# Performance work log

Hardware: AMD Instinct MI355X
Metric: run time of the kernel (lower is better)

Reference implementation:

```python
import jax, jax.numpy as jnp
import numpy as np

B, T, I, H = 1024, 96, 256, 1024


def _lin_params(key, fan_in, fan_out):
    kw, kb = jax.random.split(key)
    s = 1.0 / np.sqrt(fan_in)
    W = jax.random.uniform(kw, (fan_in, fan_out), jnp.float32, -s, s)
    b = jax.random.uniform(kb, (fan_out,), jnp.float32, -s, s)
    return W, b


def setup_inputs() -> dict:
    key = jax.random.key(0)
    ks = jax.random.split(key, 16)
    x = jax.random.normal(ks[0], (B, T, I), jnp.float32)
    mask = (jax.random.uniform(ks[1], (B, T, I)) > 0.2).astype(jnp.float32)
    delta = jax.random.uniform(ks[2], (B, T, I), jnp.float32)
    noise = jax.random.normal(ks[3], (B, T, I), jnp.float32) * 0.01
    d = {"x": x, "mask": mask, "delta": delta, "noise": noise}
    # encoder params
    d["enc_Wtd"], d["enc_btd"] = _lin_params(ks[4], I, H)
    d["enc_Wr"], d["enc_br"] = _lin_params(ks[5], H + I, H)
    d["enc_Wmu"], d["enc_bmu"] = _lin_params(ks[6], H + I, H)
    d["enc_Whh"], d["enc_bhh"] = _lin_params(ks[7], H + I, H)
    # latent + decoder-input projections
    d["z_W"], d["z_b"] = _lin_params(ks[8], H, H)
    d["di_W"], d["di_b"] = _lin_params(ks[9], H, I)
    # decoder params
    d["dec_Wtd"], d["dec_btd"] = _lin_params(ks[10], I, H)
    d["dec_Wr"], d["dec_br"] = _lin_params(ks[11], H + I, H)
    d["dec_Wmu"], d["dec_bmu"] = _lin_params(ks[12], H + I, H)
    d["dec_Whh"], d["dec_bhh"] = _lin_params(ks[13], H + I, H)
    d["reg_W"], d["reg_b"] = _lin_params(ks[14], H, I)
    return d


def _grui_cell(h, x_t, d_t, Wtd, btd, Wr, br, Wmu, bmu, Whh, bhh):
    # temporal decay gate: exp(-relu(Lin(delta_t)))
    beta = jnp.exp(-jax.nn.relu(d_t @ Wtd + btd))  # [B,H]
    h = beta * h
    hx = jnp.concatenate([h, x_t], axis=1)          # [B,H+I]
    r = jax.nn.sigmoid(hx @ Wr + br)
    mu = jax.nn.sigmoid(hx @ Wmu + bmu)
    rhx = jnp.concatenate([r * h, x_t], axis=1)
    h_hat = jnp.tanh(rhx @ Whh + bhh)
    return (1.0 - mu) * h + mu * h_hat


def reference(x, mask, delta, noise,
              enc_Wtd, enc_btd, enc_Wr, enc_br, enc_Wmu, enc_bmu, enc_Whh, enc_bhh,
              z_W, z_b, di_W, di_b,
              dec_Wtd, dec_btd, dec_Wr, dec_br, dec_Wmu, dec_bmu, dec_Whh, dec_bhh,
              reg_W, reg_b):
    xin = x * mask + noise                            # [B,T,I]
    xs = jnp.swapaxes(xin, 0, 1)                      # [T,B,I]
    ds = jnp.swapaxes(delta, 0, 1)                    # [T,B,I]
    h0 = jnp.zeros((x.shape[0], enc_Wr.shape[1]), x.dtype)

    # ---- encoder scan (dropout = identity in eval) ----
    def enc_step(h, td):
        x_t, d_t = td
        h = _grui_cell(h, x_t, d_t, enc_Wtd, enc_btd, enc_Wr, enc_br,
                       enc_Wmu, enc_bmu, enc_Whh, enc_bhh)
        return h, None

    h_enc, _ = jax.lax.scan(enc_step, h0, (xs, ds))

    z = h_enc @ z_W + z_b
    dec_in = z @ di_W + di_b                          # [B,I]

    # ---- decoder scan: carries (h, x_t), emits x_t after reg_out ----
    def dec_step(carry, d_t):
        h, x_t = carry
        h = _grui_cell(h, x_t, d_t, dec_Wtd, dec_btd, dec_Wr, dec_br,
                       dec_Wmu, dec_bmu, dec_Whh, dec_bhh)
        x_next = jnp.tanh(h @ reg_W + reg_b)
        return (h, x_next), x_next

    _, outs = jax.lax.scan(dec_step, (h0, dec_in), ds)  # outs: [T,B,I]
    return jnp.swapaxes(outs, 0, 1)                     # [B,T,I]
```

## Files before the change

kernel.cpp:

```cpp
#include <hip/hip_runtime.h>
#include <cstdint>
#include <cstddef>

#define B_ 1024
#define T_ 96
#define I_ 256
#define H_ 1024

typedef unsigned short u16;
typedef __attribute__((ext_vector_type(8))) short short8;
typedef __attribute__((ext_vector_type(4))) float f32x4;
typedef __attribute__((ext_vector_type(4))) unsigned int u32x4;

__device__ __forceinline__ float bf2f(u16 u) {
  union { unsigned int i; float f; } v;
  v.i = ((unsigned int)u) << 16;
  return v.f;
}
__device__ __forceinline__ u16 f2bf(float f) {
  union { float f; unsigned int i; } v;
  v.f = f;
  unsigned int u = v.i;
  return (u16)((u + 0x7FFFu + ((u >> 16) & 1u)) >> 16);
}
// ... 10 lines not shown
  atomicAdd(&cnt, c);
  __syncthreads();
  if (threadIdx.x == 0) *flag = (cnt > 32) ? 1 : 0;
}

__global__ void zero_f32(float* __restrict__ p, int n) {
  int i = blockIdx.x * 256 + threadIdx.x;
  if (i < n) p[i] = 0.f;
}

__global__ void transpose_w(const void* __restrict__ W, u16* __restrict__ Th,
                            u16* __restrict__ Tl, int K, int N,
                            const int* __restrict__ dflag) {
  __shared__ float tile[32][33];
  const int f = *dflag;
  int n0 = blockIdx.x * 32, k0 = blockIdx.y * 32;
  int tx = threadIdx.x, ty = threadIdx.y;
#pragma unroll
  for (int i = ty; i < 32; i += 8) {
    size_t o = (size_t)(k0 + i) * N + n0 + tx;
    tile[i][tx] = f ? ((const float*)W)[o] : bf2f(((const u16*)W)[o]);
  }
  __syncthreads();
#pragma unroll
  for (int i = ty; i < 32; i += 8) {
    float v = tile[tx][i];
    u16 h = f2bf(v);
    size_t o = (size_t)(n0 + i) * K + k0 + tx;
    Th[o] = h;
    Tl[o] = f2bf(v - bf2f(h));
  }
}

__global__ void ew_reg(float* __restrict__ P, const void* __restrict__ bias,
                       float* __restrict__ Xt, void* __restrict__ out, int t,
                       const int* __restrict__ dflag) {
  const int f = *dflag;
  int i = blockIdx.x * 256 + threadIdx.x;
  int col = i & (I_ - 1);
  int row = i >> 8;
  float bv = f ? ((const float*)bias)[col] : bf2f(((const u16*)bias)[col]);
  float v = tanhf(P[i] + bv);
  Xt[i] = v;
  size_t oidx = (size_t)row * (T_ * I_) + (size_t)t * I_ + col;
  if (f) ((float*)out)[oidx] = v;
  else ((u16*)out)[oidx] = f2bf(v);
  P[i] = 0.f;
}

template <int BN, int EPI, int AMODE>
__global__ __launch_bounds__(256) void gemm_k(
    const void* __restrict__ A0, int lda0, int aoff0, int K0,
    const void* __restrict__ Ax, const void* __restrict__ Am,
    const void* __restrict__ An, int lda1, int aoff1,
    const u16* __restrict__ BTh, const u16* __restrict__ BTl, int K, int Ksl,
    const void* __restrict__ bias0, const void* __restrict__ bias1,
    const float* __restrict__ src0, const float* __restrict__ src1,
    float* __restrict__ dst0, int dstr0, float* __restrict__ dst1,
    const int* __restrict__ dflag) {
  __shared__ __align__(16) u16 As_hi[64][40];
  __shared__ __align__(16) u16 As_lo[64][40];
  __shared__ __align__(16) u16 Bs_hi[BN][40];
  __shared__ __align__(16) u16 Bs_lo[BN][40];

  const int f = *dflag;
  const bool alo = (AMODE != 0) || f;

  const int tid = threadIdx.x;
  const int m0 = blockIdx.y * 64;
  const int n0 = blockIdx.x * BN;
  const int kbeg = blockIdx.z * Ksl;
  const int kend = kbeg + Ksl;

  const int w = tid >> 6;
  const int lane = tid & 63;
  const int wx = w & 1, wy = w >> 1;
  const int lr = lane & 15, q = lane >> 4;
  constexpr int NB = BN / 32;

  f32x4 acc[2][NB];
#pragma unroll
  for (int mb = 0; mb < 2; ++mb)
#pragma unroll
    for (int nb = 0; nb < NB; ++nb)
      acc[mb][nb] = (f32x4){0.f, 0.f, 0.f, 0.f};

  const int ar = tid >> 2, ac8 = (tid & 3) * 8;
  const int bn = (BN == 128) ? (tid >> 1) : (tid >> 2);
  const int bc = (BN == 128) ? ((tid & 1) * 16) : ((tid & 3) * 8);

  float av[8];
  u32x4 pbh0, pbh1, pbl0, pbl1;

  auto load_chunk = [&](int kc) {
    if (AMODE == 0) {
      size_t o = (size_t)(m0 + ar) * lda0 + aoff0 + kc + ac8;
      if (f) {
        f32x4 t0 = *(const f32x4*)((const float*)A0 + o);
        f32x4 t1 = *(const f32x4*)((const float*)A0 + o + 4);
#pragma unroll
        for (int j = 0; j < 4; ++j) { av[j] = t0[j]; av[j + 4] = t1[j]; }
      } else {
        union { u32x4 v; u16 s[8]; } t;
        t.v = *(const u32x4*)((const u16*)A0 + o);
#pragma unroll
        for (int j = 0; j < 8; ++j) av[j] = bf2f(t.s[j]);
      }
    } else if (kc < K0) {
      const float* Af = (const float*)A0 + (size_t)(m0 + ar) * lda0 + kc + ac8;
      f32x4 t0 = *(const f32x4*)Af;
      f32x4 t1 = *(const f32x4*)(Af + 4);
#pragma unroll
      for (int j = 0; j < 4; ++j) { av[j] = t0[j]; av[j + 4] = t1[j]; }
    } else if (AMODE == 1) {
      const float* Af = (const float*)Ax + (size_t)(m0 + ar) * lda1 + (kc - K0) + ac8;
      f32x4 t0 = *(const f32x4*)Af;
      f32x4 t1 = *(const f32x4*)(Af + 4);
#pragma unroll
      for (int j = 0; j < 4; ++j) { av[j] = t0[j]; av[j + 4] = t1[j]; }
    } else {
      size_t o = (size_t)(m0 + ar) * lda1 + aoff1 + (kc - K0) + ac8;
      if (f) {
        const float* xp = (const float*)Ax + o;
        const float* mp = (const float*)Am + o;
        const float* np = (const float*)An + o;
        f32x4 x0 = *(const f32x4*)xp, x1 = *(const f32x4*)(xp + 4);
        f32x4 m0v = *(const f32x4*)mp, m1v = *(const f32x4*)(mp + 4);
        f32x4 n0v = *(const f32x4*)np, n1v = *(const f32x4*)(np + 4);
#pragma unroll
        for (int j = 0; j < 4; ++j) {
          av[j] = x0[j] * m0v[j] + n0v[j];
          av[j + 4] = x1[j] * m1v[j] + n1v[j];
        }
      } else {
        union { u32x4 v; u16 s[8]; } ux, um, un;
        ux.v = *(const u32x4*)((const u16*)Ax + o);
        um.v = *(const u32x4*)((const u16*)Am + o);
        un.v = *(const u32x4*)((const u16*)An + o);
#pragma unroll
        for (int j = 0; j < 8; ++j)
          av[j] = bf2f(ux.s[j]) * bf2f(um.s[j]) + bf2f(un.s[j]);
      }
    }
    const u16* Bph = BTh + (size_t)(n0 + bn) * K + kc + bc;
    pbh0 = *(const u32x4*)Bph;
    if (BN == 128) pbh1 = *(const u32x4*)(Bph + 8);
    if (f) {
      const u16* Bpl = BTl + (size_t)(n0 + bn) * K + kc + bc;
      pbl0 = *(const u32x4*)Bpl;
      if (BN == 128) pbl1 = *(const u32x4*)(Bpl + 8);
    }
  };

  load_chunk(kbeg);

  for (int kc = kbeg; kc < kend; kc += 32) {
    {
      union { u16 s[8]; u32x4 v; } ph, pl;
#pragma unroll
      for (int j = 0; j < 8; ++j) {
        u16 h = f2bf(av[j]);
        ph.s[j] = h;
        pl.s[j] = f2bf(av[j] - bf2f(h));
      }
      *(u32x4*)&As_hi[ar][ac8] = ph.v;
      if (alo) *(u32x4*)&As_lo[ar][ac8] = pl.v;
    }
    *(u32x4*)&Bs_hi[bn][bc] = pbh0;
    if (BN == 128) *(u32x4*)&Bs_hi[bn][bc + 8] = pbh1;
    if (f) {
      *(u32x4*)&Bs_lo[bn][bc] = pbl0;
      if (BN == 128) *(u32x4*)&Bs_lo[bn][bc + 8] = pbl1;
    }
    __syncthreads();

    if (kc + 32 < kend) load_chunk(kc + 32);

    short8 ah[2], al[2];
#pragma unroll
    for (int mb = 0; mb < 2; ++mb) {
      ah[mb] = *(const short8*)&As_hi[wy * 32 + mb * 16 + lr][q * 8];
      if (alo) al[mb] = *(const short8*)&As_lo[wy * 32 + mb * 16 + lr][q * 8];
    }
#pragma unroll
    for (int nb = 0; nb < NB; ++nb) {
      short8 bh = *(const short8*)&Bs_hi[wx * (BN / 2) + nb * 16 + lr][q * 8];
#pragma unroll
      for (int mb = 0; mb < 2; ++mb) {
        acc[mb][nb] = __builtin_amdgcn_mfma_f32_16x16x32_bf16(ah[mb], bh, acc[mb][nb], 0, 0, 0);
        if (alo)
          acc[mb][nb] = __builtin_amdgcn_mfma_f32_16x16x32_bf16(al[mb], bh, acc[mb][nb], 0, 0, 0);
      }
      if (f) {
        short8 bl = *(const short8*)&Bs_lo[wx * (BN / 2) + nb * 16 + lr][q * 8];
#pragma unroll
        for (int mb = 0; mb < 2; ++mb)
          acc[mb][nb] = __builtin_amdgcn_mfma_f32_16x16x32_bf16(ah[mb], bl, acc[mb][nb], 0, 0, 0);
      }
    }
    __syncthreads();
  }

  auto bget = [&](const void* b, int c) -> float {
    return f ? ((const float*)b)[c] : bf2f(((const u16*)b)[c]);
  };

#pragma unroll
  for (int mb = 0; mb < 2; ++mb) {
#pragma unroll
    for (int nb = 0; nb < NB; ++nb) {
#pragma unroll
      for (int r = 0; r < 4; ++r) {
        int row = m0 + wy * 32 + mb * 16 + q * 4 + r;
        int col = n0 + wx * (BN / 2) + nb * 16 + lr;
        float p = acc[mb][nb][r];
        if (EPI == 0) {
          dst0[(size_t)row * dstr0 + col] = p + bget(bias0, col);
        } else if (EPI == 1) {
          float tt = p + bget(bias0, col);
          float beta = expf(-fmaxf(tt, 0.f));
          dst0[(size_t)row * H_ + col] = beta * src0[(size_t)row * H_ + col];
        } else if (EPI == 2) {
          if (col < H_) {
            float rr = 1.f / (1.f + expf(-(p + bget(bias0, col))));
            dst0[(size_t)row * H_ + col] = rr * src0[(size_t)row * H_ + col];
          } else {
            int c = col - H_;
            float mu = 1.f / (1.f + expf(-(p + bget(bias1, c))));
            dst1[(size_t)row * H_ + c] = mu;
          }
        } else if (EPI == 3) {
          float hh = tanhf(p + bget(bias0, col));
          float mu = src1[(size_t)row * H_ + col];
          float hs = src0[(size_t)row * H_ + col];
          dst0[(size_t)row * H_ + col] = (1.f - mu) * hs + mu * hh;
        } else if (EPI == 4) {
          atomicAdd(&dst0[(size_t)row * dstr0 + col], p);
        }
      }
    }
  }
}

extern "C" void kernel_launch(void* const* d_in, const int* in_sizes, int n_in,
                              void* d_out, int out_size, void* d_ws, size_t ws_size,
                              hipStream_t stream) {
  const void* x_ = d_in[0];
  const void* mask_ = d_in[1];
  const void* delta_ = d_in[2];
  const void* noise_ = d_in[3];
  const void* eWtd = d_in[4];
  const void* ebtd = d_in[5];
  const void* eWr = d_in[6];
  const void* ebr = d_in[7];
  const void* eWmu = d_in[8];
  const void* ebmu = d_in[9];
  const void* eWhh = d_in[10];
  const void* ebhh = d_in[11];
  const void* zW = d_in[12];
  const void* zb = d_in[13];
  const void* diW = d_in[14];
  const void* dib = d_in[15];
  const void* dWtd = d_in[16];
  const void* dbtd = d_in[17];
  const void* dWr = d_in[18];
  const void* dbr = d_in[19];
  const void* dWmu = d_in[20];
  const void* dbmu = d_in[21];
  const void* dWhh = d_in[22];
  const void* dbhh = d_in[23];
  const void* rW = d_in[24];
  const void* rb = d_in[25];

  char* ws = (char*)d_ws;
  size_t off = 0;
  auto alloc = [&](size_t bytes) -> char* {
    char* p = ws + off;
    off = (off + bytes + 255) & ~(size_t)255;
    return p;
  };
  int* dflag = (int*)alloc(256);
  float* Hb = (float*)alloc((size_t)B_ * H_ * 4);
  float* Hs = (float*)alloc((size_t)B_ * H_ * 4);
  float* RH = (float*)alloc((size_t)B_ * H_ * 4);
  float* MUb = (float*)alloc((size_t)B_ * H_ * 4);
  float* Xt = (float*)alloc((size_t)B_ * I_ * 4);
  float* Pr = (float*)alloc((size_t)B_ * I_ * 4);
  auto wpair = [&](size_t elems, u16** lo) -> u16* {
    u16* hi = (u16*)alloc(elems * 2);
    *lo = (u16*)alloc(elems * 2);
    return hi;
  };
  u16 *eWtdL, *eWrmL, *eWhhL, *zWL, *diWL, *dWtdL, *dWrmL, *dWhhL, *rWL;
  u16* eWtdT = wpair((size_t)H_ * I_, &eWtdL);
  u16* eWrmT = wpair((size_t)2 * H_ * (H_ + I_), &eWrmL);
  u16* eWhhT = wpair((size_t)H_ * (H_ + I_), &eWhhL);
  u16* zWT = wpair((size_t)H_ * H_, &zWL);
  u16* diWT = wpair((size_t)I_ * H_, &diWL);
  u16* dWtdT = wpair((size_t)H_ * I_, &dWtdL);
  u16* dWrmT = wpair((size_t)2 * H_ * (H_ + I_), &dWrmL);
  u16* dWhhT = wpair((size_t)H_ * (H_ + I_), &dWhhL);
  u16* rWT = wpair((size_t)I_ * H_, &rWL);

  detect_dtype<<<1, 256, 0, stream>>>((const u16*)x_, dflag);
  zero_f32<<<(B_ * H_) / 256, 256, 0, stream>>>(Hb, B_ * H_);
  zero_f32<<<(B_ * I_) / 256, 256, 0, stream>>>(Pr, B_ * I_);

  auto tr = [&](const void* W, u16* Th, u16* Tl, int K, int N) {
    transpose_w<<<dim3(N / 32, K / 32), dim3(32, 8), 0, stream>>>(W, Th, Tl, K, N, dflag);
  };
  tr(eWtd, eWtdT, eWtdL, I_, H_);
  tr(eWr, eWrmT, eWrmL, H_ + I_, H_);
  tr(eWmu, eWrmT + (size_t)H_ * (H_ + I_), eWrmL + (size_t)H_ * (H_ + I_), H_ + I_, H_);
  tr(eWhh, eWhhT, eWhhL, H_ + I_, H_);
  tr(zW, zWT, zWL, H_, H_);
  tr(diW, diWT, diWL, H_, I_);
  tr(dWtd, dWtdT, dWtdL, I_, H_);
  tr(dWr, dWrmT, dWrmL, H_ + I_, H_);
  tr(dWmu, dWrmT + (size_t)H_ * (H_ + I_), dWrmL + (size_t)H_ * (H_ + I_), H_ + I_, H_);
  tr(dWhh, dWhhT, dWhhL, H_ + I_, H_);
  tr(rW, rWT, rWL, H_, I_);

  const int GY = B_ / 64;

  for (int t = 0; t < T_; ++t) {
    gemm_k<64, 1, 0><<<dim3(H_ / 64, GY, 1), 256, 0, stream>>>(
        delta_, T_ * I_, t * I_, I_, nullptr, nullptr, nullptr, 0, 0,
        eWtdT, eWtdL, I_, I_, ebtd, nullptr, Hb, nullptr, Hs, H_, nullptr, dflag);
    gemm_k<128, 2, 2><<<dim3((2 * H_) / 128, GY, 1), 256, 0, stream>>>(
        Hs, H_, 0, H_, x_, mask_, noise_, T_ * I_, t * I_,
        eWrmT, eWrmL, H_ + I_, H_ + I_, ebr, ebmu, Hs, nullptr, RH, H_, MUb, dflag);
    gemm_k<64, 3, 2><<<dim3(H_ / 64, GY, 1), 256, 0, stream>>>(
        RH, H_, 0, H_, x_, mask_, noise_, T_ * I_, t * I_,
        eWhhT, eWhhL, H_ + I_, H_ + I_, ebhh, nullptr, Hs, MUb, Hb, H_, nullptr, dflag);
  }

  gemm_k<128, 0, 1><<<dim3(H_ / 128, GY, 1), 256, 0, stream>>>(
      Hb, H_, 0, H_, Hb, nullptr, nullptr, H_, 0,
      zWT, zWL, H_, H_, zb, nullptr, nullptr, nullptr, RH, H_, nullptr, dflag);
  gemm_k<128, 0, 1><<<dim3(I_ / 128, GY, 1), 256, 0, stream>>>(
      RH, H_, 0, H_, RH, nullptr, nullptr, H_, 0,
      diWT, diWL, H_, H_, dib, nullptr, nullptr, nullptr, Xt, I_, nullptr, dflag);
  zero_f32<<<(B_ * H_) / 256, 256, 0, stream>>>(Hb, B_ * H_);

  for (int t = 0; t < T_; ++t) {
    gemm_k<64, 1, 0><<<dim3(H_ / 64, GY, 1), 256, 0, stream>>>(
        delta_, T_ * I_, t * I_, I_, nullptr, nullptr, nullptr, 0, 0,
        dWtdT, dWtdL, I_, I_, dbtd, nullptr, Hb, nullptr, Hs, H_, nullptr, dflag);
    gemm_k<128, 2, 1><<<dim3((2 * H_) / 128, GY, 1), 256, 0, stream>>>(
        Hs, H_, 0, H_, Xt, nullptr, nullptr, I_, 0,
        dWrmT, dWrmL, H_ + I_, H_ + I_, dbr, dbmu, Hs, nullptr, RH, H_, MUb, dflag);
    gemm_k<64, 3, 1><<<dim3(H_ / 64, GY, 1), 256, 0, stream>>>(
        RH, H_, 0, H_, Xt, nullptr, nullptr, I_, 0,
        dWhhT, dWhhL, H_ + I_, H_ + I_, dbhh, nullptr, Hs, MUb, Hb, H_, nullptr, dflag);
    gemm_k<64, 4, 1><<<dim3(I_ / 64, GY, 4), 256, 0, stream>>>(
        Hb, H_, 0, H_, Hb, nullptr, nullptr, H_, 0,
        rWT, rWL, H_, H_ / 4, nullptr, nullptr, nullptr, nullptr, Pr, I_, nullptr, dflag);
    ew_reg<<<(B_ * I_) / 256, 256, 0, stream>>>(Pr, rb, Xt, d_out, t, dflag);
  }
}
```

Baseline: 21.08 ms.

## Precompute decay gates for all timesteps, fuse beta into gate GEMMs, drop split-K reg

Hoists the delta-to-beta projection out of both scans into one large batched GEMM over all B*T rows (when workspace allows), and applies beta inside the r/mu and candidate GEMM loaders and epilogues instead of materialising a decayed hidden state each step. Precomputes the masked-noisy input once, and replaces the split-K atomic regression GEMM plus elementwise tanh kernel with a single GEMM whose epilogue writes the output directly. The GEMM main loop is restructured to double-buffer register prefetch. This removes per-step kernel launches and redundant work, at the cost of a large extra workspace buffer, recomputing beta*h in the loads, and a regression GEMM with fewer blocks.

Result: slower. 23.62 ms (+12.0%).

```diff
diff --git a/kernel.cpp b/kernel.cpp
--- a/kernel.cpp
+++ b/kernel.cpp
@@ -66,31 +66,49 @@
   }
 }
 
-__global__ void ew_reg(float* __restrict__ P, const void* __restrict__ bias,
-                       float* __restrict__ Xt, void* __restrict__ out, int t,
-                       const int* __restrict__ dflag) {
+__global__ void make_xin(const void* __restrict__ x, const void* __restrict__ m,
+                         const void* __restrict__ nz, float* __restrict__ o,
+                         const int* __restrict__ dflag) {
   const int f = *dflag;
-  int i = blockIdx.x * 256 + threadIdx.x;
-  int col = i & (I_ - 1);
-  int row = i >> 8;
-  float bv = f ? ((const float*)bias)[col] : bf2f(((const u16*)bias)[col]);
-  float v = tanhf(P[i] + bv);
-  Xt[i] = v;
-  size_t oidx = (size_t)row * (T_ * I_) + (size_t)t * I_ + col;
-  if (f) ((float*)out)[oidx] = v;
-  else ((u16*)out)[oidx] = f2bf(v);
-  P[i] = 0.f;
-}
-
-template <int BN, int EPI, int AMODE>
+  size_t i = ((size_t)blockIdx.x * 256 + threadIdx.x) * 8;
+  float v[8];
+  if (f) {
+    const float* xp = (const float*)x + i;
+    const float* mp = (const float*)m + i;
+    const float* np = (const float*)nz + i;
+    f32x4 x0 = *(const f32x4*)xp, x1 = *(const f32x4*)(xp + 4);
+    f32x4 m0 = *(const f32x4*)mp, m1 = *(const f32x4*)(mp + 4);
+    f32x4 n0 = *(const f32x4*)np, n1 = *(const f32x4*)(np + 4);
+#pragma unroll
+    for (int j = 0; j < 4; ++j) {
+      v[j] = x0[j] * m0[j] + n0[j];
+      v[j + 4] = x1[j] * m1[j] + n1[j];
+    }
+  } else {
+    union { u32x4 q; u16 s[8]; } ux, um, un;
+    ux.q = *(const u32x4*)((const u16*)x + i);
+    um.q = *(const u32x4*)((const u16*)m + i);
+    un.q = *(const u32x4*)((const u16*)nz + i);
+#pragma unroll
+    for (int j = 0; j < 8; ++j) v[j] = bf2f(ux.s[j]) * bf2f(um.s[j]) + bf2f(un.s[j]);
+  }
+  f32x4 o0, o1;
+#pragma unroll
+  for (int j = 0; j < 4; ++j) { o0[j] = v[j]; o1[j] = v[j + 4]; }
+  *(f32x4*)(o + i) = o0;
+  *(f32x4*)(o + i + 4) = o1;
+}
+
+template <int BN, int EPI, int AH, int AI>
 __global__ __launch_bounds__(256) void gemm_k(
     const void* __restrict__ A0, int lda0, int aoff0, int K0,
     const void* __restrict__ Ax, const void* __restrict__ Am,
     const void* __restrict__ An, int lda1, int aoff1,
-    const u16* __restrict__ BTh, const u16* __restrict__ BTl, int K, int Ksl,
+    const float* Bet, int bstr,
+    const u16* __restrict__ BTh, const u16* __restrict__ BTl, int K,
     const void* __restrict__ bias0, const void* __restrict__ bias1,
-    const float* __restrict__ src0, const float* __restrict__ src1,
-    float* __restrict__ dst0, int dstr0, float* __restrict__ dst1,
+    const float* src0, const float* __restrict__ src1,
+    float* dst0, int dstr0, void* __restrict__ dst1, int tstep,
     const int* __restrict__ dflag) {
   __shared__ __align__(16) u16 As_hi[64][40];
   __shared__ __align__(16) u16 As_lo[64][40];
@@ -98,13 +116,11 @@
   __shared__ __align__(16) u16 Bs_lo[BN][40];
 
   const int f = *dflag;
-  const bool alo = (AMODE != 0) || f;
+  const bool alo = (AH != 0) || f;
 
   const int tid = threadIdx.x;
   const int m0 = blockIdx.y * 64;
   const int n0 = blockIdx.x * BN;
-  const int kbeg = blockIdx.z * Ksl;
-  const int kend = kbeg + Ksl;
 
   const int w = tid >> 6;
   const int lane = tid & 63;
@@ -123,93 +139,101 @@
   const int bn = (BN == 128) ? (tid >> 1) : (tid >> 2);
   const int bc = (BN == 128) ? ((tid & 1) * 16) : ((tid & 3) * 8);
 
-  float av[8];
-  u32x4 pbh0, pbh1, pbl0, pbl1;
-
-  auto load_chunk = [&](int kc) {
-    if (AMODE == 0) {
-      size_t o = (size_t)(m0 + ar) * lda0 + aoff0 + kc + ac8;
-      if (f) {
+  auto load_chunk = [&](int kc, float (&av)[8], u32x4 (&pbh)[2], u32x4 (&pbl)[2]) {
+    if (AI == 0 || kc < K0) {
+      if (AH == 0) {
+        size_t o = (size_t)(m0 + ar) * lda0 + aoff0 + kc + ac8;
+        if (f) {
+          f32x4 t0 = *(const f32x4*)((const float*)A0 + o);
+          f32x4 t1 = *(const f32x4*)((const float*)A0 + o + 4);
+#pragma unroll
+          for (int j = 0; j < 4; ++j) { av[j] = t0[j]; av[j + 4] = t1[j]; }
+        } else {
+          union { u32x4 v; u16 s[8]; } t;
+          t.v = *(const u32x4*)((const u16*)A0 + o);
+#pragma unroll
+          for (int j = 0; j < 8; ++j) av[j] = bf2f(t.s[j]);
+        }
+      } else if (AH == 1) {
+        size_t o = (size_t)(m0 + ar) * lda0 + aoff0 + kc + ac8;
         f32x4 t0 = *(const f32x4*)((const float*)A0 + o);
         f32x4 t1 = *(const f32x4*)((const float*)A0 + o + 4);
 #pragma unroll
         for (int j = 0; j < 4; ++j) { av[j] = t0[j]; av[j + 4] = t1[j]; }
       } else {
-        union { u32x4 v; u16 s[8]; } t;
-        t.v = *(const u32x4*)((const u16*)A0 + o);
-#pragma unroll
-        for (int j = 0; j < 8; ++j) av[j] = bf2f(t.s[j]);
+        size_t ob = (size_t)(m0 + ar) * bstr + kc + ac8;
+        size_t oh = (size_t)(m0 + ar) * H_ + kc + ac8;
+        f32x4 b0 = *(const f32x4*)(Bet + ob);
+        f32x4 b1 = *(const f32x4*)(Bet + ob + 4);
+        f32x4 h0 = *(const f32x4*)((const float*)A0 + oh);
+        f32x4 h1 = *(const f32x4*)((const float*)A0 + oh + 4);
+#pragma unroll
+        for (int j = 0; j < 4; ++j) {
+          av[j] = b0[j] * h0[j];
+          av[j + 4] = b1[j] * h1[j];
+        }
       }
-    } else if (kc < K0) {
-      const float* Af = (const float*)A0 + (size_t)(m0 + ar) * lda0 + kc + ac8;
-      f32x4 t0 = *(const f32x4*)Af;
-      f32x4 t1 = *(const f32x4*)(Af + 4);
-#pragma unroll
-      for (int j = 0; j < 4; ++j) { av[j] = t0[j]; av[j + 4] = t1[j]; }
-    } else if (AMODE == 1) {
-      const float* Af = (const float*)Ax + (size_t)(m0 + ar) * lda1 + (kc - K0) + ac8;
-      f32x4 t0 = *(const f32x4*)Af;
-      f32x4 t1 = *(const f32x4*)(Af + 4);
-#pragma unroll
-      for (int j = 0; j < 4; ++j) { av[j] = t0[j]; av[j + 4] = t1[j]; }
     } else {
-      size_t o = (size_t)(m0 + ar) * lda1 + aoff1 + (kc - K0) + ac8;
-      if (f) {
-        const float* xp = (const float*)Ax + o;
-        const float* mp = (const float*)Am + o;
-        const float* np = (const float*)An + o;
-        f32x4 x0 = *(const f32x4*)xp, x1 = *(const f32x4*)(xp + 4);
-        f32x4 m0v = *(const f32x4*)mp, m1v = *(const f32x4*)(mp + 4);
-        f32x4 n0v = *(const f32x4*)np, n1v = *(const f32x4*)(np + 4);
-#pragma unroll
-        for (int j = 0; j < 4; ++j) {
-          av[j] = x0[j] * m0v[j] + n0v[j];
-          av[j + 4] = x1[j] * m1v[j] + n1v[j];
+      int kk = kc - K0;
+      size_t o = (size_t)(m0 + ar) * lda1 + aoff1 + kk + ac8;
+      if (AI == 1) {
+        f32x4 t0 = *(const f32x4*)((const float*)Ax + o);
+        f32x4 t1 = *(const f32x4*)((const float*)Ax + o + 4);
+#pragma unroll
+        for (int j = 0; j < 4; ++j) { av[j] = t0[j]; av[j + 4] = t1[j]; }
+      } else {
+        if (f) {
+          const float* xp = (const float*)Ax + o;
+          const float* mp = (const float*)Am + o;
+          const float* np = (const float*)An + o;
+          f32x4 x0 = *(const f32x4*)xp, x1 = *(const f32x4*)(xp + 4);
+          f32x4 m0v = *(const f32x4*)mp, m1v = *(const f32x4*)(mp + 4);
+          f32x4 n0v = *(const f32x4*)np, n1v = *(const f32x4*)(np + 4);
+#pragma unroll
+          for (int j = 0; j < 4; ++j) {
+            av[j] = x0[j] * m0v[j] + n0v[j];
+            av[j + 4] = x1[j] * m1v[j] + n1v[j];
+          }
+        } else {
+          union { u32x4 v; u16 s[8]; } ux, um, un;
+          ux.v = *(const u32x4*)((const u16*)Ax + o);
+          um.v = *(const u32x4*)((const u16*)Am + o);
+          un.v = *(const u32x4*)((const u16*)An + o);
+#pragma unroll
+          for (int j = 0; j < 8; ++j)
+            av[j] = bf2f(ux.s[j]) * bf2f(um.s[j]) + bf2f(un.s[j]);
         }
-      } else {
-        union { u32x4 v; u16 s[8]; } ux, um, un;
-        ux.v = *(const u32x4*)((const u16*)Ax + o);
-        um.v = *(const u32x4*)((const u16*)Am + o);
-        un.v = *(const u32x4*)((const u16*)An + o);
-#pragma unroll
-        for (int j = 0; j < 8; ++j)
-          av[j] = bf2f(ux.s[j]) * bf2f(um.s[j]) + bf2f(un.s[j]);
       }
     }
     const u16* Bph = BTh + (size_t)(n0 + bn) * K + kc + bc;
-    pbh0 = *(const u32x4*)Bph;
-    if (BN == 128) pbh1 = *(const u32x4*)(Bph + 8);
+    pbh[0] = *(const u32x4*)Bph;
+    if (BN == 128) pbh[1] = *(const u32x4*)(Bph + 8);
     if (f) {
       const u16* Bpl = BTl + (size_t)(n0 + bn) * K + kc + bc;
-      pbl0 = *(const u32x4*)Bpl;
-      if (BN == 128) pbl1 = *(const u32x4*)(Bpl + 8);
-    }
-  };
-
-  load_chunk(kbeg);
-
-  for (int kc = kbeg; kc < kend; kc += 32) {
-    {
-      union { u16 s[8]; u32x4 v; } ph, pl;
-#pragma unroll
-      for (int j = 0; j < 8; ++j) {
-        u16 h = f2bf(av[j]);
-        ph.s[j] = h;
-        pl.s[j] = f2bf(av[j] - bf2f(h));
-      }
-      *(u32x4*)&As_hi[ar][ac8] = ph.v;
-      if (alo) *(u32x4*)&As_lo[ar][ac8] = pl.v;
-    }
-    *(u32x4*)&Bs_hi[bn][bc] = pbh0;
-    if (BN == 128) *(u32x4*)&Bs_hi[bn][bc + 8] = pbh1;
+      pbl[0] = *(const u32x4*)Bpl;
+      if (BN == 128) pbl[1] = *(const u32x4*)(Bpl + 8);
+    }
+  };
+
+  auto drain = [&](float (&av)[8], u32x4 (&pbh)[2], u32x4 (&pbl)[2]) {
+    union { u16 s[8]; u32x4 v; } ph, pl;
+#pragma unroll
+    for (int j = 0; j < 8; ++j) {
+      u16 h = f2bf(av[j]);
+      ph.s[j] = h;
+      pl.s[j] = f2bf(av[j] - bf2f(h));
+    }
+    *(u32x4*)&As_hi[ar][ac8] = ph.v;
+    if (alo) *(u32x4*)&As_lo[ar][ac8] = pl.v;
+    *(u32x4*)&Bs_hi[bn][bc] = pbh[0];
+    if (BN == 128) *(u32x4*)&Bs_hi[bn][bc + 8] = pbh[1];
     if (f) {
-      *(u32x4*)&Bs_lo[bn][bc] = pbl0;
-      if (BN == 128) *(u32x4*)&Bs_lo[bn][bc + 8] = pbl1;
-    }
-    __syncthreads();
-
-    if (kc + 32 < kend) load_chunk(kc + 32);
-
+      *(u32x4*)&Bs_lo[bn][bc] = pbl[0];
+      if (BN == 128) *(u32x4*)&Bs_lo[bn][bc + 8] = pbl[1];
+    }
+  };
+
+  auto mfma_phase = [&]() {
     short8 ah[2], al[2];
 #pragma unroll
     for (int mb = 0; mb < 2; ++mb) {
@@ -232,7 +256,25 @@
           acc[mb][nb] = __builtin_amdgcn_mfma_f32_16x16x32_bf16(ah[mb], bl, acc[mb][nb], 0, 0, 0);
       }
     }
+  };
+
+  float av0[8], av1[8];
+  u32x4 bh0[2], bl0[2], bh1[2], bl1[2];
+  load_chunk(0, av0, bh0, bl0);
+  if (32 < K) load_chunk(32, av1, bh1, bl1);
+  for (int kc = 0; kc < K; kc += 64) {
+    drain(av0, bh0, bl0);
     __syncthreads();
+    if (kc + 64 < K) load_chunk(kc + 64, av0, bh0, bl0);
+    mfma_phase();
+    __syncthreads();
+    if (kc + 32 < K) {
+      drain(av1, bh1, bl1);
+      __syncthreads();
+      if (kc + 96 < K) load_chunk(kc + 96, av1, bh1, bl1);
+      mfma_phase();
+      __syncthreads();
+    }
   }
 
   auto bget = [&](const void* b, int c) -> float {
@@ -250,26 +292,30 @@
         float p = acc[mb][nb][r];
         if (EPI == 0) {
           dst0[(size_t)row * dstr0 + col] = p + bget(bias0, col);
-        } else if (EPI == 1) {
-          float tt = p + bget(bias0, col);
-          float beta = expf(-fmaxf(tt, 0.f));
-          dst0[(size_t)row * H_ + col] = beta * src0[(size_t)row * H_ + col];
         } else if (EPI == 2) {
           if (col < H_) {
             float rr = 1.f / (1.f + expf(-(p + bget(bias0, col))));
-            dst0[(size_t)row * H_ + col] = rr * src0[(size_t)row * H_ + col];
+            dst0[(size_t)row * H_ + col] =
+                rr * Bet[(size_t)row * bstr + col] * src0[(size_t)row * H_ + col];
           } else {
             int c = col - H_;
             float mu = 1.f / (1.f + expf(-(p + bget(bias1, c))));
-            dst1[(size_t)row * H_ + c] = mu;
+            ((float*)dst1)[(size_t)row * H_ + c] = mu;
           }
         } else if (EPI == 3) {
+          size_t ix = (size_t)row * H_ + col;
           float hh = tanhf(p + bget(bias0, col));
-          float mu = src1[(size_t)row * H_ + col];
-          float hs = src0[(size_t)row * H_ + col];
-          dst0[(size_t)row * H_ + col] = (1.f - mu) * hs + mu * hh;
-        } else if (EPI == 4) {
-          atomicAdd(&dst0[(size_t)row * dstr0 + col], p);
+          float mu = src1[ix];
+          float hs = Bet[(size_t)row * bstr + col] * src0[ix];
+          dst0[ix] = (1.f - mu) * hs + mu * hh;
+        } else if (EPI == 5) {
+          float v = tanhf(p + bget(bias0, col));
+          dst0[(size_t)row * dstr0 + col] = v;
+          size_t ox = (size_t)row * (T_ * I_) + (size_t)tstep * I_ + col;
+          if (f) ((float*)dst1)[ox] = v;
+          else ((u16*)dst1)[ox] = f2bf(v);
+        } else if (EPI == 7) {
+          dst0[(size_t)row * dstr0 + col] = expf(-fmaxf(p + bget(bias0, col), 0.f));
         }
       }
     }
@@ -315,11 +361,10 @@
   };
   int* dflag = (int*)alloc(256);
   float* Hb = (float*)alloc((size_t)B_ * H_ * 4);
-  float* Hs = (float*)alloc((size_t)B_ * H_ * 4);
   float* RH = (float*)alloc((size_t)B_ * H_ * 4);
   float* MUb = (float*)alloc((size_t)B_ * H_ * 4);
   float* Xt = (float*)alloc((size_t)B_ * I_ * 4);
-  float* Pr = (float*)alloc((size_t)B_ * I_ * 4);
+  float* Beta1 = (float*)alloc((size_t)B_ * H_ * 4);
   auto wpair = [&](size_t elems, u16** lo) -> u16* {
     u16* hi = (u16*)alloc(elems * 2);
     *lo = (u16*)alloc(elems * 2);
@@ -335,10 +380,15 @@
   u16* dWrmT = wpair((size_t)2 * H_ * (H_ + I_), &dWrmL);
   u16* dWhhT = wpair((size_t)H_ * (H_ + I_), &dWhhL);
   u16* rWT = wpair((size_t)I_ * H_, &rWL);
+  float* Xin = (float*)alloc((size_t)B_ * T_ * I_ * 4);
+  size_t xin_end = off;
+  float* BetaT = (float*)alloc((size_t)B_ * T_ * H_ * 4);
+  size_t full_end = off;
+  const bool xinT = ws_size >= xin_end;
+  const bool fullT = ws_size >= full_end;
 
   detect_dtype<<<1, 256, 0, stream>>>((const u16*)x_, dflag);
   zero_f32<<<(B_ * H_) / 256, 256, 0, stream>>>(Hb, B_ * H_);
-  zero_f32<<<(B_ * I_) / 256, 256, 0, stream>>>(Pr, B_ * I_);
 
   auto tr = [&](const void* W, u16* Th, u16* Tl, int K, int N) {
     transpose_w<<<dim3(N / 32, K / 32), dim3(32, 8), 0, stream>>>(W, Th, Tl, K, N, dflag);
@@ -355,41 +405,68 @@
   tr(dWhh, dWhhT, dWhhL, H_ + I_, H_);
   tr(rW, rWT, rWL, H_, I_);
 
+  if (xinT)
+    make_xin<<<(B_ * T_ * I_) / (256 * 8), 256, 0, stream>>>(x_, mask_, noise_, Xin, dflag);
+
   const int GY = B_ / 64;
 
+  auto beta_all = [&](const u16* Th, const u16* Tl, const void* bias) {
+    gemm_k<128, 7, 0, 0><<<dim3(H_ / 128, (B_ * T_) / 64), 256, 0, stream>>>(
+        delta_, I_, 0, I_, nullptr, nullptr, nullptr, 0, 0, nullptr, 0,
+        Th, Tl, I_, bias, nullptr, nullptr, nullptr, BetaT, H_, nullptr, 0, dflag);
+  };
+  auto beta_step = [&](const u16* Th, const u16* Tl, const void* bias, int t) {
+    gemm_k<128, 7, 0, 0><<<dim3(H_ / 128, GY), 256, 0, stream>>>(
+        delta_, T_ * I_, t * I_, I_, nullptr, nullptr, nullptr, 0, 0, nullptr, 0,
+        Th, Tl, I_, bias, nullptr, nullptr, nullptr, Beta1, H_, nullptr, 0, dflag);
+  };
+
+  if (fullT) beta_all(eWtdT, eWtdL, ebtd);
   for (int t = 0; t < T_; ++t) {
-    gemm_k<64, 1, 0><<<dim3(H_ / 64, GY, 1), 256, 0, stream>>>(
-        delta_, T_ * I_, t * I_, I_, nullptr, nullptr, nullptr, 0, 0,
-        eWtdT, eWtdL, I_, I_, ebtd, nullptr, Hb, nullptr, Hs, H_, nullptr, dflag);
-    gemm_k<128, 2, 2><<<dim3((2 * H_) / 128, GY, 1), 256, 0, stream>>>(
-        Hs, H_, 0, H_, x_, mask_, noise_, T_ * I_, t * I_,
-        eWrmT, eWrmL, H_ + I_, H_ + I_, ebr, ebmu, Hs, nullptr, RH, H_, MUb, dflag);
-    gemm_k<64, 3, 2><<<dim3(H_ / 64, GY, 1), 256, 0, stream>>>(
-        RH, H_, 0, H_, x_, mask_, noise_, T_ * I_, t * I_,
-        eWhhT, eWhhL, H_ + I_, H_ + I_, ebhh, nullptr, Hs, MUb, Hb, H_, nullptr, dflag);
-  }
-
-  gemm_k<128, 0, 1><<<dim3(H_ / 128, GY, 1), 256, 0, stream>>>(
-      Hb, H_, 0, H_, Hb, nullptr, nullptr, H_, 0,
-      zWT, zWL, H_, H_, zb, nullptr, nullptr, nullptr, RH, H_, nullptr, dflag);
-  gemm_k<128, 0, 1><<<dim3(I_ / 128, GY, 1), 256, 0, stream>>>(
-      RH, H_, 0, H_, RH, nullptr, nullptr, H_, 0,
-      diWT, diWL, H_, H_, dib, nullptr, nullptr, nullptr, Xt, I_, nullptr, dflag);
+    const float* Bet;
+    int bstr;
+    if (fullT) { Bet = BetaT + (size_t)t * H_; bstr = T_ * H_; }
+    else { beta_step(eWtdT, eWtdL, ebtd, t); Bet = Beta1; bstr = H_; }
+    if (xinT)
+      gemm_k<128, 2, 2, 1><<<dim3((2 * H_) / 128, GY), 256, 0, stream>>>(
+          Hb, H_, 0, H_, Xin, nullptr, nullptr, T_ * I_, t * I_, Bet, bstr,
+          eWrmT, eWrmL, H_ + I_, ebr, ebmu, Hb, nullptr, RH, H_, MUb, 0, dflag);
+    else
+      gemm_k<128, 2, 2, 2><<<dim3((2 * H_) / 128, GY), 256, 0, stream>>>(
+          Hb, H_, 0, H_, x_, mask_, noise_, T_ * I_, t * I_, Bet, bstr,
+          eWrmT, eWrmL, H_ + I_, ebr, ebmu, Hb, nullptr, RH, H_, MUb, 0, dflag);
+    if (xinT)
+      gemm_k<64, 3, 1, 1><<<dim3(H_ / 64, GY), 256, 0, stream>>>(
+          RH, H_, 0, H_, Xin, nullptr, nullptr, T_ * I_, t * I_, Bet, bstr,
+          eWhhT, eWhhL, H_ + I_, ebhh, nullptr, Hb, MUb, Hb, H_, nullptr, 0, dflag);
+    else
+      gemm_k<64, 3, 1, 2><<<dim3(H_ / 64, GY), 256, 0, stream>>>(
+          RH, H_, 0, H_, x_, mask_, noise_, T_ * I_, t * I_, Bet, bstr,
+          eWhhT, eWhhL, H_ + I_, ebhh, nullptr, Hb, MUb, Hb, H_, nullptr, 0, dflag);
+  }
+
+  gemm_k<128, 0, 1, 0><<<dim3(H_ / 128, GY), 256, 0, stream>>>(
+      Hb, H_, 0, H_, nullptr, nullptr, nullptr, 0, 0, nullptr, 0,
+      zWT, zWL, H_, zb, nullptr, nullptr, nullptr, RH, H_, nullptr, 0, dflag);
+  gemm_k<128, 0, 1, 0><<<dim3(I_ / 128, GY), 256, 0, stream>>>(
+      RH, H_, 0, H_, nullptr, nullptr, nullptr, 0, 0, nullptr, 0,
+      diWT, diWL, H_, dib, nullptr, nullptr, nullptr, Xt, I_, nullptr, 0, dflag);
   zero_f32<<<(B_ * H_) / 256, 256, 0, stream>>>(Hb, B_ * H_);
 
+  if (fullT) beta_all(dWtdT, dWtdL, dbtd);
   for (int t = 0; t < T_; ++t) {
-    gemm_k<64, 1, 0><<<dim3(H_ / 64, GY, 1), 256, 0, stream>>>(
-        delta_, T_ * I_, t * I_, I_, nullptr, nullptr, nullptr, 0, 0,
-        dWtdT, dWtdL, I_, I_, dbtd, nullptr, Hb, nullptr, Hs, H_, nullptr, dflag);
-    gemm_k<128, 2, 1><<<dim3((2 * H_) / 128, GY, 1), 256, 0, stream>>>(
-        Hs, H_, 0, H_, Xt, nullptr, nullptr, I_, 0,
-        dWrmT, dWrmL, H_ + I_, H_ + I_, dbr, dbmu, Hs, nullptr, RH, H_, MUb, dflag);
-    gemm_k<64, 3, 1><<<dim3(H_ / 64, GY, 1), 256, 0, stream>>>(
-        RH, H_, 0, H_, Xt, nullptr, nullptr, I_, 0,
-        dWhhT, dWhhL, H_ + I_, H_ + I_, dbhh, nullptr, Hs, MUb, Hb, H_, nullptr, dflag);
-    gemm_k<64, 4, 1><<<dim3(I_ / 64, GY, 4), 256, 0, stream>>>(
-        Hb, H_, 0, H_, Hb, nullptr, nullptr, H_, 0,
-        rWT, rWL, H_, H_ / 4, nullptr, nullptr, nullptr, nullptr, Pr, I_, nullptr, dflag);
-    ew_reg<<<(B_ * I_) / 256, 256, 0, stream>>>(Pr, rb, Xt, d_out, t, dflag);
-  }
-}
+    const float* Bet;
+    int bstr;
+    if (fullT) { Bet = BetaT + (size_t)t * H_; bstr = T_ * H_; }
+    else { beta_step(dWtdT, dWtdL, dbtd, t); Bet = Beta1; bstr = H_; }
+    gemm_k<128, 2, 2, 1><<<dim3((2 * H_) / 128, GY), 256, 0, stream>>>(
+        Hb, H_, 0, H_, Xt, nullptr, nullptr, I_, 0, Bet, bstr,
+        dWrmT, dWrmL, H_ + I_, dbr, dbmu, Hb, nullptr, RH, H_, MUb, 0, dflag);
+    gemm_k<64, 3, 1, 1><<<dim3(H_ / 64, GY), 256, 0, stream>>>(
+        RH, H_, 0, H_, Xt, nullptr, nullptr, I_, 0, Bet, bstr,
+        dWhhT, dWhhL, H_ + I_, dbhh, nullptr, Hb, MUb, Hb, H_, nullptr, 0, dflag);
+    gemm_k<64, 5, 1, 0><<<dim3(I_ / 64, GY), 256, 0, stream>>>(
+        Hb, H_, 0, H_, nullptr, nullptr, nullptr, 0, 0, nullptr, 0,
+        rWT, rWL, H_, rb, nullptr, nullptr, nullptr, Xt, I_, d_out, t, dflag);
+  }
+}
```

## Store intermediate activations as pre-split bf16 hi/lo planes for GEMM operands

Applied to the files above, without the earlier changes.

Intermediate activations (scaled hidden state, r*h, decoder input) are now written by GEMM epilogues directly as bf16 hi/lo plane pairs, so the next GEMM copies them straight into shared memory instead of loading fp32 and splitting in the inner loop. A one-time kernel also precomputes x*mask+noise as hi/lo planes for the whole sequence, when workspace allows, which removes the per-step triple loads and FMA. The aim is to cut per-chunk conversion ALU work and halve activation load bytes. It costs extra workspace and an upfront pass over the full input tensor. It also keeps a fallback path for when the workspace is too small.

Measured after the change: 20.11 ms. 4.6% less time.

```diff
diff --git a/kernel.cpp b/kernel.cpp
--- a/kernel.cpp
+++ b/kernel.cpp
@@ -66,8 +66,46 @@
   }
 }
 
+__global__ void make_xin_planes(const void* __restrict__ x, const void* __restrict__ m,
+                                const void* __restrict__ nz, u16* __restrict__ oh,
+                                u16* __restrict__ ol, const int* __restrict__ dflag) {
+  const int f = *dflag;
+  size_t i = ((size_t)blockIdx.x * 256 + threadIdx.x) * 8;
+  float v[8];
+  if (f) {
+    const float* xp = (const float*)x + i;
+    const float* mp = (const float*)m + i;
+    const float* np = (const float*)nz + i;
+    f32x4 x0 = *(const f32x4*)xp, x1 = *(const f32x4*)(xp + 4);
+    f32x4 m0 = *(const f32x4*)mp, m1 = *(const f32x4*)(mp + 4);
+    f32x4 n0 = *(const f32x4*)np, n1 = *(const f32x4*)(np + 4);
+#pragma unroll
+    for (int j = 0; j < 4; ++j) {
+      v[j] = x0[j] * m0[j] + n0[j];
+      v[j + 4] = x1[j] * m1[j] + n1[j];
+    }
+  } else {
+    union { u32x4 q; u16 s[8]; } ux, um, un;
+    ux.q = *(const u32x4*)((const u16*)x + i);
+    um.q = *(const u32x4*)((const u16*)m + i);
+    un.q = *(const u32x4*)((const u16*)nz + i);
+#pragma unroll
+    for (int j = 0; j < 8; ++j) v[j] = bf2f(ux.s[j]) * bf2f(um.s[j]) + bf2f(un.s[j]);
+  }
+  union { u16 s[8]; u32x4 q; } ph, pl;
+#pragma unroll
+  for (int j = 0; j < 8; ++j) {
+    u16 h = f2bf(v[j]);
+    ph.s[j] = h;
+    pl.s[j] = f2bf(v[j] - bf2f(h));
+  }
+  *(u32x4*)(oh + i) = ph.q;
+  *(u32x4*)(ol + i) = pl.q;
+}
+
 __global__ void ew_reg(float* __restrict__ P, const void* __restrict__ bias,
-                       float* __restrict__ Xt, void* __restrict__ out, int t,
+                       u16* __restrict__ XtH, u16* __restrict__ XtL,
+                       void* __restrict__ out, int t,
                        const int* __restrict__ dflag) {
   const int f = *dflag;
   int i = blockIdx.x * 256 + threadIdx.x;
@@ -75,7 +113,9 @@
   int row = i >> 8;
   float bv = f ? ((const float*)bias)[col] : bf2f(((const u16*)bias)[col]);
   float v = tanhf(P[i] + bv);
-  Xt[i] = v;
+  u16 h = f2bf(v);
+  XtH[i] = h;
+  XtL[i] = f2bf(v - bf2f(h));
   size_t oidx = (size_t)row * (T_ * I_) + (size_t)t * I_ + col;
   if (f) ((float*)out)[oidx] = v;
   else ((u16*)out)[oidx] = f2bf(v);
@@ -84,13 +124,16 @@
 
 template <int BN, int EPI, int AMODE>
 __global__ __launch_bounds__(256) void gemm_k(
-    const void* __restrict__ A0, int lda0, int aoff0, int K0,
+    const void* __restrict__ A0, const void* __restrict__ Al, int lda0,
+    int aoff0, int K0,
     const void* __restrict__ Ax, const void* __restrict__ Am,
     const void* __restrict__ An, int lda1, int aoff1,
     const u16* __restrict__ BTh, const u16* __restrict__ BTl, int K, int Ksl,
     const void* __restrict__ bias0, const void* __restrict__ bias1,
     const float* __restrict__ src0, const float* __restrict__ src1,
+    const u16* __restrict__ sph, const u16* __restrict__ spl,
     float* __restrict__ dst0, int dstr0, float* __restrict__ dst1,
+    u16* __restrict__ dph, u16* __restrict__ dpl,
     const int* __restrict__ dflag) {
   __shared__ __align__(16) u16 As_hi[64][40];
   __shared__ __align__(16) u16 As_lo[64][40];
@@ -124,6 +167,7 @@
   const int bc = (BN == 128) ? ((tid & 1) * 16) : ((tid & 3) * 8);
 
   float av[8];
+  u32x4 pah, pal;
   u32x4 pbh0, pbh1, pbl0, pbl1;
 
   auto load_chunk = [&](int kc) {
@@ -135,45 +179,52 @@
 #pragma unroll
         for (int j = 0; j < 4; ++j) { av[j] = t0[j]; av[j + 4] = t1[j]; }
       } else {
-        union { u32x4 v; u16 s[8]; } t;
-        t.v = *(const u32x4*)((const u16*)A0 + o);
-#pragma unroll
-        for (int j = 0; j < 8; ++j) av[j] = bf2f(t.s[j]);
+        pah = *(const u32x4*)((const u16*)A0 + o);
       }
     } else if (kc < K0) {
-      const float* Af = (const float*)A0 + (size_t)(m0 + ar) * lda0 + kc + ac8;
-      f32x4 t0 = *(const f32x4*)Af;
-      f32x4 t1 = *(const f32x4*)(Af + 4);
-#pragma unroll
-      for (int j = 0; j < 4; ++j) { av[j] = t0[j]; av[j + 4] = t1[j]; }
-    } else if (AMODE == 1) {
-      const float* Af = (const float*)Ax + (size_t)(m0 + ar) * lda1 + (kc - K0) + ac8;
-      f32x4 t0 = *(const f32x4*)Af;
-      f32x4 t1 = *(const f32x4*)(Af + 4);
-#pragma unroll
-      for (int j = 0; j < 4; ++j) { av[j] = t0[j]; av[j + 4] = t1[j]; }
+      size_t o = (size_t)(m0 + ar) * lda0 + aoff0 + kc + ac8;
+      if (AMODE == 1 || AMODE == 2) {
+        f32x4 t0 = *(const f32x4*)((const float*)A0 + o);
+        f32x4 t1 = *(const f32x4*)((const float*)A0 + o + 4);
+#pragma unroll
+        for (int j = 0; j < 4; ++j) { av[j] = t0[j]; av[j + 4] = t1[j]; }
+      } else {
+        pah = *(const u32x4*)((const u16*)A0 + o);
+        pal = *(const u32x4*)((const u16*)Al + o);
+      }
     } else {
-      size_t o = (size_t)(m0 + ar) * lda1 + aoff1 + (kc - K0) + ac8;
-      if (f) {
-        const float* xp = (const float*)Ax + o;
-        const float* mp = (const float*)Am + o;
-        const float* np = (const float*)An + o;
-        f32x4 x0 = *(const f32x4*)xp, x1 = *(const f32x4*)(xp + 4);
-        f32x4 m0v = *(const f32x4*)mp, m1v = *(const f32x4*)(mp + 4);
-        f32x4 n0v = *(const f32x4*)np, n1v = *(const f32x4*)(np + 4);
-#pragma unroll
-        for (int j = 0; j < 4; ++j) {
-          av[j] = x0[j] * m0v[j] + n0v[j];
-          av[j + 4] = x1[j] * m1v[j] + n1v[j];
+      int kk = kc - K0;
+      size_t o = (size_t)(m0 + ar) * lda1 + aoff1 + kk + ac8;
+      if (AMODE == 1) {
+        f32x4 t0 = *(const f32x4*)((const float*)Ax + o);
+        f32x4 t1 = *(const f32x4*)((const float*)Ax + o + 4);
+#pragma unroll
+        for (int j = 0; j < 4; ++j) { av[j] = t0[j]; av[j + 4] = t1[j]; }
+      } else if (AMODE == 3) {
+        pah = *(const u32x4*)((const u16*)Ax + o);
+        pal = *(const u32x4*)((const u16*)Am + o);
+      } else {
+        if (f) {
+          const float* xp = (const float*)Ax + o;
+          const float* mp = (const float*)Am + o;
+          const float* np = (const float*)An + o;
+          f32x4 x0 = *(const f32x4*)xp, x1 = *(const f32x4*)(xp + 4);
+          f32x4 m0v = *(const f32x4*)mp, m1v = *(const f32x4*)(mp + 4);
+          f32x4 n0v = *(const f32x4*)np, n1v = *(const f32x4*)(np + 4);
+#pragma unroll
+          for (int j = 0; j < 4; ++j) {
+            av[j] = x0[j] * m0v[j] + n0v[j];
+            av[j + 4] = x1[j] * m1v[j] + n1v[j];
+          }
+        } else {
+          union { u32x4 v; u16 s[8]; } ux, um, un;
+          ux.v = *(const u32x4*)((const u16*)Ax + o);
+          um.v = *(const u32x4*)((const u16*)Am + o);
+          un.v = *(const u32x4*)((const u16*)An + o);
+#pragma unroll
+          for (int j = 0; j < 8; ++j)
+            av[j] = bf2f(ux.s[j]) * bf2f(um.s[j]) + bf2f(un.s[j]);
         }
-      } else {
-        union { u32x4 v; u16 s[8]; } ux, um, un;
-        ux.v = *(const u32x4*)((const u16*)Ax + o);
-        um.v = *(const u32x4*)((const u16*)Am + o);
-        un.v = *(const u32x4*)((const u16*)An + o);
-#pragma unroll
-        for (int j = 0; j < 8; ++j)
-          av[j] = bf2f(ux.s[j]) * bf2f(um.s[j]) + bf2f(un.s[j]);
       }
     }
     const u16* Bph = BTh + (size_t)(n0 + bn) * K + kc + bc;
@@ -186,10 +237,12 @@
     }
   };
 
-  load_chunk(kbeg);
-
-  for (int kc = kbeg; kc < kend; kc += 32) {
-    {
+  auto drain = [&](int kc) {
+    bool plane = (AMODE == 3) || (AMODE == 4 && kc < K0) || (AMODE == 0 && !f);
+    if (plane) {
+      *(u32x4*)&As_hi[ar][ac8] = pah;
+      if (AMODE != 0) *(u32x4*)&As_lo[ar][ac8] = pal;
+    } else {
       union { u16 s[8]; u32x4 v; } ph, pl;
 #pragma unroll
       for (int j = 0; j < 8; ++j) {
@@ -206,6 +259,12 @@
       *(u32x4*)&Bs_lo[bn][bc] = pbl0;
       if (BN == 128) *(u32x4*)&Bs_lo[bn][bc + 8] = pbl1;
     }
+  };
+
+  load_chunk(kbeg);
+
+  for (int kc = kbeg; kc < kend; kc += 32) {
+    drain(kc);
     __syncthreads();
 
     if (kc + 32 < kend) load_chunk(kc + 32);
@@ -237,6 +296,11 @@
 
   auto bget = [&](const void* b, int c) -> float {
     return f ? ((const float*)b)[c] : bf2f(((const u16*)b)[c]);
+  };
+  auto pstore = [&](size_t ix, float v) {
+    u16 h = f2bf(v);
+    dph[ix] = h;
+    dpl[ix] = f2bf(v - bf2f(h));
   };
 
 #pragma unroll
@@ -251,25 +315,29 @@
         if (EPI == 0) {
           dst0[(size_t)row * dstr0 + col] = p + bget(bias0, col);
         } else if (EPI == 1) {
-          float tt = p + bget(bias0, col);
-          float beta = expf(-fmaxf(tt, 0.f));
-          dst0[(size_t)row * H_ + col] = beta * src0[(size_t)row * H_ + col];
+          float beta = expf(-fmaxf(p + bget(bias0, col), 0.f));
+          pstore((size_t)row * H_ + col, beta * src0[(size_t)row * H_ + col]);
         } else if (EPI == 2) {
           if (col < H_) {
+            size_t ix = (size_t)row * H_ + col;
             float rr = 1.f / (1.f + expf(-(p + bget(bias0, col))));
-            dst0[(size_t)row * H_ + col] = rr * src0[(size_t)row * H_ + col];
+            float hs = bf2f(sph[ix]) + bf2f(spl[ix]);
+            pstore(ix, rr * hs);
           } else {
             int c = col - H_;
             float mu = 1.f / (1.f + expf(-(p + bget(bias1, c))));
             dst1[(size_t)row * H_ + c] = mu;
           }
         } else if (EPI == 3) {
+          size_t ix = (size_t)row * H_ + col;
           float hh = tanhf(p + bget(bias0, col));
-          float mu = src1[(size_t)row * H_ + col];
-          float hs = src0[(size_t)row * H_ + col];
-          dst0[(size_t)row * H_ + col] = (1.f - mu) * hs + mu * hh;
+          float mu = src1[ix];
+          float hs = bf2f(sph[ix]) + bf2f(spl[ix]);
+          dst0[ix] = (1.f - mu) * hs + mu * hh;
         } else if (EPI == 4) {
           atomicAdd(&dst0[(size_t)row * dstr0 + col], p);
+        } else if (EPI == 6) {
+          pstore((size_t)row * dstr0 + col, p + bget(bias0, col));
         }
       }
     }
@@ -315,11 +383,15 @@
   };
   int* dflag = (int*)alloc(256);
   float* Hb = (float*)alloc((size_t)B_ * H_ * 4);
-  float* Hs = (float*)alloc((size_t)B_ * H_ * 4);
-  float* RH = (float*)alloc((size_t)B_ * H_ * 4);
   float* MUb = (float*)alloc((size_t)B_ * H_ * 4);
-  float* Xt = (float*)alloc((size_t)B_ * I_ * 4);
+  float* Z = (float*)alloc((size_t)B_ * H_ * 4);
   float* Pr = (float*)alloc((size_t)B_ * I_ * 4);
+  u16* HsH = (u16*)alloc((size_t)B_ * H_ * 2);
+  u16* HsL = (u16*)alloc((size_t)B_ * H_ * 2);
+  u16* RHH = (u16*)alloc((size_t)B_ * H_ * 2);
+  u16* RHL = (u16*)alloc((size_t)B_ * H_ * 2);
+  u16* XtH = (u16*)alloc((size_t)B_ * I_ * 2);
+  u16* XtL = (u16*)alloc((size_t)B_ * I_ * 2);
   auto wpair = [&](size_t elems, u16** lo) -> u16* {
     u16* hi = (u16*)alloc(elems * 2);
     *lo = (u16*)alloc(elems * 2);
@@ -335,6 +407,9 @@
   u16* dWrmT = wpair((size_t)2 * H_ * (H_ + I_), &dWrmL);
   u16* dWhhT = wpair((size_t)H_ * (H_ + I_), &dWhhL);
   u16* rWT = wpair((size_t)I_ * H_, &rWL);
+  u16* XinH = (u16*)alloc((size_t)B_ * T_ * I_ * 2);
+  u16* XinL = (u16*)alloc((size_t)B_ * T_ * I_ * 2);
+  const bool xinT = ws_size >= off;
 
   detect_dtype<<<1, 256, 0, stream>>>((const u16*)x_, dflag);
   zero_f32<<<(B_ * H_) / 256, 256, 0, stream>>>(Hb, B_ * H_);
@@ -355,41 +430,66 @@
   tr(dWhh, dWhhT, dWhhL, H_ + I_, H_);
   tr(rW, rWT, rWL, H_, I_);
 
+  if (xinT)
+    make_xin_planes<<<(B_ * T_ * I_) / (256 * 8), 256, 0, stream>>>(
+        x_, mask_, noise_, XinH, XinL, dflag);
+
   const int GY = B_ / 64;
 
   for (int t = 0; t < T_; ++t) {
     gemm_k<64, 1, 0><<<dim3(H_ / 64, GY, 1), 256, 0, stream>>>(
-        delta_, T_ * I_, t * I_, I_, nullptr, nullptr, nullptr, 0, 0,
-        eWtdT, eWtdL, I_, I_, ebtd, nullptr, Hb, nullptr, Hs, H_, nullptr, dflag);
-    gemm_k<128, 2, 2><<<dim3((2 * H_) / 128, GY, 1), 256, 0, stream>>>(
-        Hs, H_, 0, H_, x_, mask_, noise_, T_ * I_, t * I_,
-        eWrmT, eWrmL, H_ + I_, H_ + I_, ebr, ebmu, Hs, nullptr, RH, H_, MUb, dflag);
-    gemm_k<64, 3, 2><<<dim3(H_ / 64, GY, 1), 256, 0, stream>>>(
-        RH, H_, 0, H_, x_, mask_, noise_, T_ * I_, t * I_,
-        eWhhT, eWhhL, H_ + I_, H_ + I_, ebhh, nullptr, Hs, MUb, Hb, H_, nullptr, dflag);
+        delta_, nullptr, T_ * I_, t * I_, I_, nullptr, nullptr, nullptr, 0, 0,
+        eWtdT, eWtdL, I_, I_, ebtd, nullptr, Hb, nullptr, nullptr, nullptr,
+        nullptr, 0, nullptr, HsH, HsL, dflag);
+    if (xinT)
+      gemm_k<128, 2, 3><<<dim3((2 * H_) / 128, GY, 1), 256, 0, stream>>>(
+          HsH, HsL, H_, 0, H_, XinH, XinL, nullptr, T_ * I_, t * I_,
+          eWrmT, eWrmL, H_ + I_, H_ + I_, ebr, ebmu, nullptr, nullptr, HsH, HsL,
+          nullptr, 0, MUb, RHH, RHL, dflag);
+    else
+      gemm_k<128, 2, 4><<<dim3((2 * H_) / 128, GY, 1), 256, 0, stream>>>(
+          HsH, HsL, H_, 0, H_, x_, mask_, noise_, T_ * I_, t * I_,
+          eWrmT, eWrmL, H_ + I_, H_ + I_, ebr, ebmu, nullptr, nullptr, HsH, HsL,
+          nullptr, 0, MUb, RHH, RHL, dflag);
+    if (xinT)
+      gemm_k<64, 3, 3><<<dim3(H_ / 64, GY, 1), 256, 0, stream>>>(
+          RHH, RHL, H_, 0, H_, XinH, XinL, nullptr, T_ * I_, t * I_,
+          eWhhT, eWhhL, H_ + I_, H_ + I_, ebhh, nullptr, nullptr, MUb, HsH, HsL,
+          Hb, H_, nullptr, nullptr, nullptr, dflag);
+    else
+      gemm_k<64, 3, 4><<<dim3(H_ / 64, GY, 1), 256, 0, stream>>>(
+          RHH, RHL, H_, 0, H_, x_, mask_, noise_, T_ * I_, t * I_,
+          eWhhT, eWhhL, H_ + I_, H_ + I_, ebhh, nullptr, nullptr, MUb, HsH, HsL,
+          Hb, H_, nullptr, nullptr, nullptr, dflag);
   }
 
   gemm_k<128, 0, 1><<<dim3(H_ / 128, GY, 1), 256, 0, stream>>>(
-      Hb, H_, 0, H_, Hb, nullptr, nullptr, H_, 0,
-      zWT, zWL, H_, H_, zb, nullptr, nullptr, nullptr, RH, H_, nullptr, dflag);
-  gemm_k<128, 0, 1><<<dim3(I_ / 128, GY, 1), 256, 0, stream>>>(
-      RH, H_, 0, H_, RH, nullptr, nullptr, H_, 0,
-      diWT, diWL, H_, H_, dib, nullptr, nullptr, nullptr, Xt, I_, nullptr, dflag);
+      Hb, nullptr, H_, 0, H_, nullptr, nullptr, nullptr, 0, 0,
+      zWT, zWL, H_, H_, zb, nullptr, nullptr, nullptr, nullptr, nullptr,
+      Z, H_, nullptr, nullptr, nullptr, dflag);
+  gemm_k<128, 6, 1><<<dim3(I_ / 128, GY, 1), 256, 0, stream>>>(
+      Z, nullptr, H_, 0, H_, nullptr, nullptr, nullptr, 0, 0,
+      diWT, diWL, H_, H_, dib, nullptr, nullptr, nullptr, nullptr, nullptr,
+      nullptr, I_, nullptr, XtH, XtL, dflag);
   zero_f32<<<(B_ * H_) / 256, 256, 0, stream>>>(Hb, B_ * H_);
 
   for (int t = 0; t < T_; ++t) {
     gemm_k<64, 1, 0><<<dim3(H_ / 64, GY, 1), 256, 0, stream>>>(
-        delta_, T_ * I_, t * I_, I_, nullptr, nullptr, nullptr, 0, 0,
-        dWtdT, dWtdL, I_, I_, dbtd, nullptr, Hb, nullptr, Hs, H_, nullptr, dflag);
-    gemm_k<128, 2, 1><<<dim3((2 * H_) / 128, GY, 1), 256, 0, stream>>>(
-        Hs, H_, 0, H_, Xt, nullptr, nullptr, I_, 0,
-        dWrmT, dWrmL, H_ + I_, H_ + I_, dbr, dbmu, Hs, nullptr, RH, H_, MUb, dflag);
-    gemm_k<64, 3, 1><<<dim3(H_ / 64, GY, 1), 256, 0, stream>>>(
-        RH, H_, 0, H_, Xt, nullptr, nullptr, I_, 0,
-        dWhhT, dWhhL, H_ + I_, H_ + I_, dbhh, nullptr, Hs, MUb, Hb, H_, nullptr, dflag);
+        delta_, nullptr, T_ * I_, t * I_, I_, nullptr, nullptr, nullptr, 0, 0,
+        dWtdT, dWtdL, I_, I_, dbtd, nullptr, Hb, nullptr, nullptr, nullptr,
+        nullptr, 0, nullptr, HsH, HsL, dflag);
+    gemm_k<128, 2, 3><<<dim3((2 * H_) / 128, GY, 1), 256, 0, stream>>>(
+        HsH, HsL, H_, 0, H_, XtH, XtL, nullptr, I_, 0,
+        dWrmT, dWrmL, H_ + I_, H_ + I_, dbr, dbmu, nullptr, nullptr, HsH, HsL,
+        nullptr, 0, MUb, RHH, RHL, dflag);
+    gemm_k<64, 3, 3><<<dim3(H_ / 64, GY, 1), 256, 0, stream>>>(
+        RHH, RHL, H_, 0, H_, XtH, XtL, nullptr, I_, 0,
+        dWhhT, dWhhL, H_ + I_, H_ + I_, dbhh, nullptr, nullptr, MUb, HsH, HsL,
+        Hb, H_, nullptr, nullptr, nullptr, dflag);
     gemm_k<64, 4, 1><<<dim3(I_ / 64, GY, 4), 256, 0, stream>>>(
-        Hb, H_, 0, H_, Hb, nullptr, nullptr, H_, 0,
-        rWT, rWL, H_, H_ / 4, nullptr, nullptr, nullptr, nullptr, Pr, I_, nullptr, dflag);
-    ew_reg<<<(B_ * I_) / 256, 256, 0, stream>>>(Pr, rb, Xt, d_out, t, dflag);
-  }
-}
+        Hb, nullptr, H_, 0, H_, nullptr, nullptr, nullptr, 0, 0,
+        rWT, rWL, H_, H_ / 4, nullptr, nullptr, nullptr, nullptr, nullptr, nullptr,
+        Pr, I_, nullptr, nullptr, nullptr, dflag);
+    ew_reg<<<(B_ * I_) / 256, 256, 0, stream>>>(Pr, rb, XtH, XtL, d_out, t, dflag);
+  }
+}
```
